# Performance work log

Hardware: AMD Instinct MI355X
Metric: run time of the kernel (lower is better)

Reference implementation:

```python
import jax, jax.numpy as jnp
import numpy as np

CONF_THRESH = 0.01
IOU_THRESH = 0.5
K = 512          # fixed pre-NMS candidate count (top-K by confidence)
MAX_WH = 4096.0  # class offset for class-aware NMS (yolov5 style)
B, N, C = 16, 25200, 85  # batch, anchors (640x640 yolov5), 5+80 classes


def xywh2xyxy(b):
    xy, wh = b[..., :2], b[..., 2:4] * 0.5
    return jnp.concatenate([xy - wh, xy + wh], axis=-1)


def box_iou(a, b):
    # a: [M,4], b: [P,4] in xyxy -> [M,P]
    lt = jnp.maximum(a[:, None, :2], b[None, :, :2])
    rb = jnp.minimum(a[:, None, 2:], b[None, :, 2:])
    inter = jnp.clip(rb - lt, 0.0).prod(-1)
    area_a = (a[:, 2] - a[:, 0]) * (a[:, 3] - a[:, 1])
    area_b = (b[:, 2] - b[:, 0]) * (b[:, 3] - b[:, 1])
    return inter / (area_a[:, None] + area_b[None, :] - inter + 1e-9)


def _score_one(pred, target):
    # pred: [N, 85] = [xywh, obj, 80 class scores]
    obj = pred[:, 4]
    cls_conf = pred[:, 5:] * obj[:, None]            # obj * class prob
    conf = cls_conf.max(-1)
    cls = jnp.argmax(cls_conf, -1)
    boxes = xywh2xyxy(pred[:, :4])
    valid = (obj > CONF_THRESH) & (conf > CONF_THRESH)
    masked = jnp.where(valid, conf, -1.0)
    scores, order = jax.lax.top_k(masked, K)          # sorted desc, fixed K
    b = boxes[order]
    c = cls[order]
    v = scores > 0.0
    # class-aware NMS via coordinate offset
    off = b + c[:, None].astype(b.dtype) * MAX_WH
    iou = box_iou(off, off)                            # [K,K]
    idxs = jnp.arange(K)

    def body(i, keep):
        sup = jnp.any((iou[i] > IOU_THRESH) & keep & (idxs < i))
        return keep.at[i].set(v[i] & ~sup)

    keep = jax.lax.fori_loop(0, K, body, jnp.zeros(K, bool))

    tmask = keep & (c == target[5].astype(jnp.int32))  # correct-class kept boxes
    iou_t = box_iou(b, target[None, :4])[:, 0]         # IoU with target box
    m = jnp.where(tmask, iou_t, -1.0)
    j = jnp.argmax(m)
    return jnp.where(jnp.any(tmask), scores[j] * iou_t[j], 0.0)


def setup_inputs() -> dict:
    key = jax.random.key(0)
    k1, k2, k3, k4 = jax.random.split(key, 4)
    xy = jax.random.uniform(k1, (B, N, 2)) * 640.0
    wh = jax.random.uniform(k2, (B, N, 2)) * 160.0 + 4.0
    obj = jax.random.uniform(k3, (B, N, 1))
    cls = jax.random.uniform(k4, (B, N, C - 5))
    x = jnp.concatenate([xy, wh, obj, cls], axis=-1)
    target = jnp.array([120.0, 150.0, 360.0, 420.0, 0.9, 17.0], dtype=jnp.float32)
    return {"x": x, "target": target}


def reference(x, target):
    return jax.vmap(lambda p: _score_one(p, target))(x)  # [B]
```

## Files before the change

kernel.cpp:

```cpp
#include <hip/hip_runtime.h>
#include <stdint.h>

#pragma clang fp contract(off)

#define BB 16
#define NN 25200
#define CCH 85
#define KTOP 512
#define NBKT 1024
#define CAP 1024


__global__ __launch_bounds__(256) void k_conf(const float* __restrict__ x,
                                              float* __restrict__ conf) {
    __shared__ float tile[128 * CCH];
    const int blk = blockIdx.x;
    const int tid = threadIdx.x;

    const float4* src = (const float4*)x + (size_t)blk * 2720;
    float4* dst = (float4*)tile;
    for (int i = tid; i < 2720; i += 256) dst[i] = src[i];
    __syncthreads();

    const int r = tid >> 1;
    const int half = tid & 1;
    const float* row = tile + r * CCH;
    const float obj = row[4];

    float best = -1.0f;
    const float* cp = row + 5 + half * 40;
#pragma unroll
    for (int j = 0; j < 40; ++j) best = fmaxf(best, cp[j] * obj);
    best = fmaxf(best, __shfl_xor(best, 1));

    if (half == 0) {
        const int gr = blk * 128 + r;
        conf[gr] = ((obj > 0.01f) && (best > 0.01f)) ? best : -1.0f;
    }
}

__global__ __launch_bounds__(1024) void k_fused(const float* __restrict__ x,
                                                const float* __restrict__ target,
                                                const float* __restrict__ conf,
                                                float* __restrict__ out) {
    __shared__ union {
        unsigned hist[NBKT];
        unsigned mask[KTOP][16];
    } um;
    __shared__ unsigned long long cand[CAP];
    __shared__ float4 sox[KTOP];
    __shared__ float sscore[KTOP];
    __shared__ unsigned keep_words[16];
    __shared__ unsigned long long wred[16];
    __shared__ int sh_tstar, sh_cnt;

    const int b = blockIdx.x;
    const int tid = threadIdx.x;
    const int lane = tid & 63;
    const float4* cb4 = (const float4*)(conf + (size_t)b * NN);

    um.hist[tid] = 0u;
    if (tid == 0) { sh_tstar = 0; sh_cnt = 0; }
    __syncthreads();
    for (int i4 = tid; i4 < NN / 4; i4 += 1024) {
        float4 c4 = cb4[i4];
        float cs[4] = {c4.x, c4.y, c4.z, c4.w};
#pragma unroll
        for (int e = 0; e < 4; ++e) {
            float c = cs[e];
            if (c > 0.0f) {
                int bk = (int)(c * 1024.0f);
                if (bk > NBKT - 1) bk = NBKT - 1;
                atomicAdd(&um.hist[bk], 1u);
            }
        }
    }
    __syncthreads();

    for (int off = 1; off < NBKT; off <<= 1) {
        unsigned v = um.hist[tid];
        if (tid + off < NBKT) v += um.hist[tid + off];
        __syncthreads();
        um.hist[tid] = v;
        __syncthreads();
    }
    if (um.hist[tid] >= KTOP && (tid == NBKT - 1 || um.hist[tid + 1] < KTOP)) sh_tstar = tid;
    __syncthreads();
    const int tstar = sh_tstar;

    for (int i4 = tid; i4 < NN / 4; i4 += 1024) {
        float4 c4 = cb4[i4];
        float cs[4] = {c4.x, c4.y, c4.z, c4.w};
#pragma unroll
        for (int e = 0; e < 4; ++e) {
            float c = cs[e];
            bool want = false;
            if (c > 0.0f) {
                int bk = (int)(c * 1024.0f);
                if (bk > NBKT - 1) bk = NBKT - 1;
                want = (bk >= tstar);
            }
            unsigned long long bal = __ballot(want);
            int base = 0;
            if (lane == 0 && bal) base = atomicAdd(&sh_cnt, __popcll(bal));
            base = __shfl(base, 0);
            if (want) {
                int pos = base + __popcll(bal & ((1ull << lane) - 1ull));
                if (pos < CAP) {
                    unsigned bits = __float_as_uint(c);
                    cand[pos] = ((unsigned long long)bits << 32) | (unsigned)(~(i4 * 4 + e));
                }
            }
        }
    }
    __syncthreads();
    const int M = min(sh_cnt, CAP);

    unsigned long long key = (tid < M) ? cand[tid] : 0ull;
    __syncthreads();
    for (int kk = 2; kk <= CAP; kk <<= 1) {
        for (int j = kk >> 1; j > 0; j >>= 1) {
            unsigned long long partner;
            if (j >= 64) {
                cand[tid] = key;
                __syncthreads();
                partner = cand[tid ^ j];
                __syncthreads();
            } else {
                partner = __shfl_xor(key, j);
            }
            bool desc = (tid & kk) == 0;
            bool lower = (tid & j) == 0;
            bool take_max = (lower == desc);
            bool pg = partner > key;
            key = (take_max == pg) ? partner : key;
        }
    }
    cand[tid] = key;
    __syncthreads();

    const int rank = tid >> 1;
    const int half = tid & 1;
    unsigned long long rkey = cand[rank];
    float sc = __uint_as_float((unsigned)(rkey >> 32));
    unsigned idx = ~((unsigned)rkey);
    const bool v = sc > 0.0f;
    float X1 = 0.f, Y1 = 0.f, X2 = 0.f, Y2 = 0.f;
    int cl = 0;
    if (v) {
        const float* rw = x + ((size_t)b * NN + idx) * CCH;
        const float obj = rw[4];
        float bbest = -1.0f;
        int bi = 0;
        const float* cp = rw + 5 + half * 40;
#pragma unroll 8
        for (int j = 0; j < 40; ++j) {
            float p = cp[j] * obj;
            if (p > bbest) { bbest = p; bi = j; }
        }
        bi += half * 40;
        float ov = __shfl_xor(bbest, 1);
        int oi = __shfl_xor(bi, 1);
        if (half == 0) {
            if (ov > bbest) { bbest = ov; bi = oi; }
            cl = bi;
            float cx = rw[0], cy = rw[1];
            float w = rw[2] * 0.5f, h = rw[3] * 0.5f;
            X1 = cx - w; Y1 = cy - h; X2 = cx + w; Y2 = cy + h;
        }
    }
    if (half == 0) {
        sscore[rank] = sc;
        float offv = (float)cl * 4096.0f;
        sox[rank] = make_float4(X1 + offv, Y1 + offv, X2 + offv, Y2 + offv);
    }
    __syncthreads();

    for (int p = tid; p < KTOP * 16; p += 1024) {
        int i = p & (KTOP - 1);
        int w = p >> 9;
        unsigned bits = 0u;
        if ((w << 5) < i) {
            float4 bi4 = sox[i];
            float ai = (bi4.z - bi4.x) * (bi4.w - bi4.y);
            const int jbase = w << 5;
            for (int jj = 0; jj < 32; ++jj) {
                int j = jbase + jj;
                float4 bj = sox[j];
                float lx = fmaxf(bi4.x, bj.x);
                float ly = fmaxf(bi4.y, bj.y);
                float rx = fminf(bi4.z, bj.z);
                float ry = fminf(bi4.w, bj.w);
                float inter = fmaxf(rx - lx, 0.0f) * fmaxf(ry - ly, 0.0f);
                float aj = (bj.z - bj.x) * (bj.w - bj.y);
                float den = ai + aj - inter + 1e-9f;
                float iou = inter / den;
                unsigned hit = (unsigned)((j < i) & (iou > 0.5f));
                bits |= hit << jj;
            }
        }
        um.mask[i][w] = bits;
    }
    __syncthreads();

    if (tid < 64) {
        const int l15 = tid & 15;
        unsigned keepw = 0u;
        unsigned r_cur = um.mask[0][l15];
        float sc_cur = sscore[0];
        for (int i = 0; i < KTOP; ++i) {
            unsigned r_next = 0u; float sc_next = 0.f;
            if (i < KTOP - 1) { r_next = um.mask[i + 1][l15]; sc_next = sscore[i + 1]; }
            unsigned long long bal = __ballot((r_cur & keepw) != 0u);
            bool sup = (bal & 0xFFFFull) != 0ull;
            bool kept = (sc_cur > 0.0f) && !sup;
            if (kept && tid == (i >> 5)) keepw |= (1u << (i & 31));
            r_cur = r_next; sc_cur = sc_next;
        }
        if (tid < 16) keep_words[tid] = keepw;
    }
    __syncthreads();

    const float tb0 = target[0], tb1 = target[1], tb2 = target[2], tb3 = target[3];
    const int tcls = (int)target[5];
    float m = -1.0f;
    if (half == 0) {
        bool kept = (keep_words[rank >> 5] >> (rank & 31)) & 1u;
        if (kept && cl == tcls) {
            float lx = fmaxf(X1, tb0);
            float ly = fmaxf(Y1, tb1);
            float rx = fminf(X2, tb2);
            float ry = fminf(Y2, tb3);
            float inter = fmaxf(rx - lx, 0.0f) * fmaxf(ry - ly, 0.0f);
            float areab = (X2 - X1) * (Y2 - Y1);
            float areat = (tb2 - tb0) * (tb3 - tb1);
            float den = areab + areat - inter + 1e-9f;
            m = inter / den;
        }
    }
    unsigned mb = __float_as_uint(m);
    unsigned mono = (mb & 0x80000000u) ? ~mb : (mb | 0x80000000u);
    unsigned long long rk = ((unsigned long long)mono << 32) | (unsigned)(~rank);
    for (int d = 32; d > 0; d >>= 1) {
        unsigned long long o = __shfl_xor(rk, d);
        if (o > rk) rk = o;
    }
    if ((tid & 63) == 0) wred[tid >> 6] = rk;
    __syncthreads();
    if (tid == 0) {
        unsigned long long bestk = wred[0];
        for (int i = 1; i < 16; ++i)
            if (wred[i] > bestk) bestk = wred[i];
        unsigned mono2 = (unsigned)(bestk >> 32);
        unsigned mbits = (mono2 & 0x80000000u) ? (mono2 & 0x7FFFFFFFu) : ~mono2;
        float mstar = __uint_as_float(mbits);
        int j = (int)(~((unsigned)bestk));
        out[b] = (mstar >= 0.0f) ? sscore[j] * mstar : 0.0f;
    }
}

extern "C" void kernel_launch(void* const* d_in, const int* in_sizes, int n_in,
                              void* d_out, int out_size, void* d_ws, size_t ws_size,
                              hipStream_t stream) {
    const float* x = (const float*)d_in[0];
    const float* target = (const float*)d_in[1];
    float* out = (float*)d_out;
    float* conf = (float*)d_ws;

    k_conf<<<dim3((BB * NN) / 128), dim3(256), 0, stream>>>(x, conf);
    k_fused<<<dim3(BB), dim3(1024), 0, stream>>>(x, target, conf, out);
}
```

Measured before the change: 316.0 us.

## Split NMS IoU-mask stage across 128 cooperative blocks with grid syncs

Replaces the 16-block fused kernel with a cooperative 128-block kernel. Phase one is top-K selection per image on 16 blocks, now with a shuffle-based histogram scan. Those blocks write boxes, scores and classes to global workspace. After a grid sync, 8 blocks per image each compute a slice of the K×K IoU suppression bitmask, reusing precomputed areas. A second grid sync hands off to the sequential greedy suppression and final target scoring, run per image with a deeper prefetch. The aim is to spread the quadratic IoU work over more CUs, at the cost of two grid-wide barriers and extra global-memory round trips.

Result: slower. 368.2 us (+16.5%).

```diff
diff --git a/kernel.cpp b/kernel.cpp
--- a/kernel.cpp
+++ b/kernel.cpp
@@ -1,4 +1,5 @@
 #include <hip/hip_runtime.h>
+#include <hip/hip_cooperative_groups.h>
 #include <stdint.h>
 
 #pragma clang fp contract(off)
@@ -10,6 +11,10 @@
 #define NBKT 1024
 #define CAP 1024
 
+#define META0 1703936
+#define SB 65536
+
+namespace cg = cooperative_groups;
 
 __global__ __launch_bounds__(256) void k_conf(const float* __restrict__ x,
                                               float* __restrict__ conf) {
@@ -39,150 +44,177 @@
     }
 }
 
-__global__ __launch_bounds__(1024) void k_fused(const float* __restrict__ x,
-                                                const float* __restrict__ target,
-                                                const float* __restrict__ conf,
-                                                float* __restrict__ out) {
+__global__ __launch_bounds__(1024) void k_rest(const float* __restrict__ x,
+                                               const float* __restrict__ target,
+                                               const float* __restrict__ conf,
+                                               char* __restrict__ meta,
+                                               float* __restrict__ out) {
     __shared__ union {
-        unsigned hist[NBKT];
+        struct { unsigned hist[NBKT]; unsigned long long cand[CAP]; } p1;
         unsigned mask[KTOP][16];
     } um;
-    __shared__ unsigned long long cand[CAP];
     __shared__ float4 sox[KTOP];
+    __shared__ float sarea[KTOP];
     __shared__ float sscore[KTOP];
+    __shared__ int scls[KTOP];
+    __shared__ unsigned wsum[16];
     __shared__ unsigned keep_words[16];
     __shared__ unsigned long long wred[16];
     __shared__ int sh_tstar, sh_cnt;
 
-    const int b = blockIdx.x;
+    cg::grid_group grid = cg::this_grid();
     const int tid = threadIdx.x;
     const int lane = tid & 63;
-    const float4* cb4 = (const float4*)(conf + (size_t)b * NN);
-
-    um.hist[tid] = 0u;
-    if (tid == 0) { sh_tstar = 0; sh_cnt = 0; }
-    __syncthreads();
-    for (int i4 = tid; i4 < NN / 4; i4 += 1024) {
-        float4 c4 = cb4[i4];
-        float cs[4] = {c4.x, c4.y, c4.z, c4.w};
+    const int bid = blockIdx.x;
+
+    if (bid < BB) {
+        const int b = bid;
+        char* mb = meta + (size_t)b * SB;
+        const float4* cb4 = (const float4*)(conf + (size_t)b * NN);
+
+        um.p1.hist[tid] = 0u;
+        if (tid == 0) { sh_tstar = 0; sh_cnt = 0; }
+        __syncthreads();
+        for (int i4 = tid; i4 < NN / 4; i4 += 1024) {
+            float4 c4 = cb4[i4];
+            float cs[4] = {c4.x, c4.y, c4.z, c4.w};
 #pragma unroll
-        for (int e = 0; e < 4; ++e) {
-            float c = cs[e];
-            if (c > 0.0f) {
-                int bk = (int)(c * 1024.0f);
-                if (bk > NBKT - 1) bk = NBKT - 1;
-                atomicAdd(&um.hist[bk], 1u);
-            }
+            for (int e = 0; e < 4; ++e) {
+                float c = cs[e];
+                if (c > 0.0f) {
+                    int bk = (int)(c * 1024.0f);
+                    if (bk > NBKT - 1) bk = NBKT - 1;
+                    atomicAdd(&um.p1.hist[bk], 1u);
+                }
+            }
+        }
+        __syncthreads();
+
+        unsigned v = um.p1.hist[tid];
+        unsigned s = v;
+#pragma unroll
+        for (int d = 1; d < 64; d <<= 1) {
+            unsigned t = __shfl_down(s, d);
+            if (lane + d < 64) s += t;
+        }
+        if (lane == 0) wsum[tid >> 6] = s;
+        __syncthreads();
+        unsigned off = 0;
+        for (int w = (tid >> 6) + 1; w < 16; ++w) off += wsum[w];
+        unsigned S = s + off;
+        if (S >= KTOP && (S - v) < KTOP) sh_tstar = tid;
+        __syncthreads();
+        const int tstar = sh_tstar;
+
+        for (int i4 = tid; i4 < NN / 4; i4 += 1024) {
+            float4 c4 = cb4[i4];
+            float cs[4] = {c4.x, c4.y, c4.z, c4.w};
+#pragma unroll
+            for (int e = 0; e < 4; ++e) {
+                float c = cs[e];
+                bool want = false;
+                if (c > 0.0f) {
+                    int bk = (int)(c * 1024.0f);
+                    if (bk > NBKT - 1) bk = NBKT - 1;
+                    want = (bk >= tstar);
+                }
+                unsigned long long bal = __ballot(want);
+                int base = 0;
+                if (lane == 0 && bal) base = atomicAdd(&sh_cnt, __popcll(bal));
+                base = __shfl(base, 0);
+                if (want) {
+                    int pos = base + __popcll(bal & ((1ull << lane) - 1ull));
+                    if (pos < CAP) {
+                        unsigned bits = __float_as_uint(c);
+                        um.p1.cand[pos] =
+                            ((unsigned long long)bits << 32) | (unsigned)(~(i4 * 4 + e));
+                    }
+                }
+            }
+        }
+        __syncthreads();
+        const int M = min(sh_cnt, CAP);
+
+        unsigned long long key = (tid < M) ? um.p1.cand[tid] : 0ull;
+        __syncthreads();
+        for (int kk = 2; kk <= CAP; kk <<= 1) {
+            for (int j = kk >> 1; j > 0; j >>= 1) {
+                unsigned long long partner;
+                if (j >= 64) {
+                    um.p1.cand[tid] = key;
+                    __syncthreads();
+                    partner = um.p1.cand[tid ^ j];
+                    __syncthreads();
+                } else {
+                    partner = __shfl_xor(key, j);
+                }
+                bool desc = (tid & kk) == 0;
+                bool lower = (tid & j) == 0;
+                bool take_max = (lower == desc);
+                bool pg = partner > key;
+                key = (take_max == pg) ? partner : key;
+            }
+        }
+        um.p1.cand[tid] = key;
+        __syncthreads();
+
+        const int rank = tid >> 1;
+        const int half = tid & 1;
+        unsigned long long rkey = um.p1.cand[rank];
+        float sc = __uint_as_float((unsigned)(rkey >> 32));
+        unsigned idx = ~((unsigned)rkey);
+        const bool v2 = sc > 0.0f;
+        float X1 = 0.f, Y1 = 0.f, X2 = 0.f, Y2 = 0.f;
+        int cl = 0;
+        if (v2) {
+            const float* rw = x + ((size_t)b * NN + idx) * CCH;
+            const float obj = rw[4];
+            float bbest = -1.0f;
+            int bi = 0;
+            const float* cp = rw + 5 + half * 40;
+#pragma unroll 8
+            for (int j = 0; j < 40; ++j) {
+                float p = cp[j] * obj;
+                if (p > bbest) { bbest = p; bi = j; }
+            }
+            bi += half * 40;
+            float ov = __shfl_xor(bbest, 1);
+            int oi = __shfl_xor(bi, 1);
+            if (half == 0) {
+                if (ov > bbest) { bbest = ov; bi = oi; }
+                cl = bi;
+                float cx = rw[0], cy = rw[1];
+                float w = rw[2] * 0.5f, h = rw[3] * 0.5f;
+                X1 = cx - w; Y1 = cy - h; X2 = cx + w; Y2 = cy + h;
+            }
+        }
+        if (half == 0) {
+            float offv = (float)cl * 4096.0f;
+            ((float4*)mb)[rank] = make_float4(X1 + offv, Y1 + offv, X2 + offv, Y2 + offv);
+            ((float4*)(mb + 8192))[rank] = make_float4(X1, Y1, X2, Y2);
+            ((float*)(mb + 16384))[rank] = sc;
+            ((int*)(mb + 18432))[rank] = cl;
         }
     }
-    __syncthreads();
-
-    for (int off = 1; off < NBKT; off <<= 1) {
-        unsigned v = um.hist[tid];
-        if (tid + off < NBKT) v += um.hist[tid + off];
-        __syncthreads();
-        um.hist[tid] = v;
-        __syncthreads();
-    }
-    if (um.hist[tid] >= KTOP && (tid == NBKT - 1 || um.hist[tid + 1] < KTOP)) sh_tstar = tid;
-    __syncthreads();
-    const int tstar = sh_tstar;
-
-    for (int i4 = tid; i4 < NN / 4; i4 += 1024) {
-        float4 c4 = cb4[i4];
-        float cs[4] = {c4.x, c4.y, c4.z, c4.w};
-#pragma unroll
-        for (int e = 0; e < 4; ++e) {
-            float c = cs[e];
-            bool want = false;
-            if (c > 0.0f) {
-                int bk = (int)(c * 1024.0f);
-                if (bk > NBKT - 1) bk = NBKT - 1;
-                want = (bk >= tstar);
-            }
-            unsigned long long bal = __ballot(want);
-            int base = 0;
-            if (lane == 0 && bal) base = atomicAdd(&sh_cnt, __popcll(bal));
-            base = __shfl(base, 0);
-            if (want) {
-                int pos = base + __popcll(bal & ((1ull << lane) - 1ull));
-                if (pos < CAP) {
-                    unsigned bits = __float_as_uint(c);
-                    cand[pos] = ((unsigned long long)bits << 32) | (unsigned)(~(i4 * 4 + e));
-                }
-            }
-        }
-    }
-    __syncthreads();
-    const int M = min(sh_cnt, CAP);
-
-    unsigned long long key = (tid < M) ? cand[tid] : 0ull;
-    __syncthreads();
-    for (int kk = 2; kk <= CAP; kk <<= 1) {
-        for (int j = kk >> 1; j > 0; j >>= 1) {
-            unsigned long long partner;
-            if (j >= 64) {
-                cand[tid] = key;
-                __syncthreads();
-                partner = cand[tid ^ j];
-                __syncthreads();
-            } else {
-                partner = __shfl_xor(key, j);
-            }
-            bool desc = (tid & kk) == 0;
-            bool lower = (tid & j) == 0;
-            bool take_max = (lower == desc);
-            bool pg = partner > key;
-            key = (take_max == pg) ? partner : key;
-        }
-    }
-    cand[tid] = key;
-    __syncthreads();
-
-    const int rank = tid >> 1;
-    const int half = tid & 1;
-    unsigned long long rkey = cand[rank];
-    float sc = __uint_as_float((unsigned)(rkey >> 32));
-    unsigned idx = ~((unsigned)rkey);
-    const bool v = sc > 0.0f;
-    float X1 = 0.f, Y1 = 0.f, X2 = 0.f, Y2 = 0.f;
-    int cl = 0;
-    if (v) {
-        const float* rw = x + ((size_t)b * NN + idx) * CCH;
-        const float obj = rw[4];
-        float bbest = -1.0f;
-        int bi = 0;
-        const float* cp = rw + 5 + half * 40;
-#pragma unroll 8
-        for (int j = 0; j < 40; ++j) {
-            float p = cp[j] * obj;
-            if (p > bbest) { bbest = p; bi = j; }
-        }
-        bi += half * 40;
-        float ov = __shfl_xor(bbest, 1);
-        int oi = __shfl_xor(bi, 1);
-        if (half == 0) {
-            if (ov > bbest) { bbest = ov; bi = oi; }
-            cl = bi;
-            float cx = rw[0], cy = rw[1];
-            float w = rw[2] * 0.5f, h = rw[3] * 0.5f;
-            X1 = cx - w; Y1 = cy - h; X2 = cx + w; Y2 = cy + h;
-        }
-    }
-    if (half == 0) {
-        sscore[rank] = sc;
-        float offv = (float)cl * 4096.0f;
-        sox[rank] = make_float4(X1 + offv, Y1 + offv, X2 + offv, Y2 + offv);
-    }
-    __syncthreads();
-
-    for (int p = tid; p < KTOP * 16; p += 1024) {
-        int i = p & (KTOP - 1);
-        int w = p >> 9;
+    __threadfence();
+    grid.sync();
+
+    {
+        const int b = bid >> 3;
+        const int slice = bid & 7;
+        char* mb = meta + (size_t)b * SB;
+        if (tid < KTOP) {
+            float4 o = ((const float4*)mb)[tid];
+            sox[tid] = o;
+            sarea[tid] = (o.z - o.x) * (o.w - o.y);
+        }
+        __syncthreads();
+        const int i = slice * 64 + (tid >> 4);
+        const int w = tid & 15;
         unsigned bits = 0u;
         if ((w << 5) < i) {
             float4 bi4 = sox[i];
-            float ai = (bi4.z - bi4.x) * (bi4.w - bi4.y);
+            float ai = sarea[i];
             const int jbase = w << 5;
             for (int jj = 0; jj < 32; ++jj) {
                 int j = jbase + jj;
@@ -192,70 +224,84 @@
                 float rx = fminf(bi4.z, bj.z);
                 float ry = fminf(bi4.w, bj.w);
                 float inter = fmaxf(rx - lx, 0.0f) * fmaxf(ry - ly, 0.0f);
-                float aj = (bj.z - bj.x) * (bj.w - bj.y);
-                float den = ai + aj - inter + 1e-9f;
+                float den = ai + sarea[j] - inter + 1e-9f;
                 float iou = inter / den;
                 unsigned hit = (unsigned)((j < i) & (iou > 0.5f));
                 bits |= hit << jj;
             }
         }
-        um.mask[i][w] = bits;
+        ((unsigned*)(mb + 20480))[slice * 1024 + tid] = bits;
     }
-    __syncthreads();
-
-    if (tid < 64) {
-        const int l15 = tid & 15;
-        unsigned keepw = 0u;
-        unsigned r_cur = um.mask[0][l15];
-        float sc_cur = sscore[0];
-        for (int i = 0; i < KTOP; ++i) {
-            unsigned r_next = 0u; float sc_next = 0.f;
-            if (i < KTOP - 1) { r_next = um.mask[i + 1][l15]; sc_next = sscore[i + 1]; }
-            unsigned long long bal = __ballot((r_cur & keepw) != 0u);
-            bool sup = (bal & 0xFFFFull) != 0ull;
-            bool kept = (sc_cur > 0.0f) && !sup;
-            if (kept && tid == (i >> 5)) keepw |= (1u << (i & 31));
-            r_cur = r_next; sc_cur = sc_next;
-        }
-        if (tid < 16) keep_words[tid] = keepw;
-    }
-    __syncthreads();
-
-    const float tb0 = target[0], tb1 = target[1], tb2 = target[2], tb3 = target[3];
-    const int tcls = (int)target[5];
-    float m = -1.0f;
-    if (half == 0) {
-        bool kept = (keep_words[rank >> 5] >> (rank & 31)) & 1u;
-        if (kept && cl == tcls) {
-            float lx = fmaxf(X1, tb0);
-            float ly = fmaxf(Y1, tb1);
-            float rx = fminf(X2, tb2);
-            float ry = fminf(Y2, tb3);
-            float inter = fmaxf(rx - lx, 0.0f) * fmaxf(ry - ly, 0.0f);
-            float areab = (X2 - X1) * (Y2 - Y1);
-            float areat = (tb2 - tb0) * (tb3 - tb1);
-            float den = areab + areat - inter + 1e-9f;
-            m = inter / den;
-        }
-    }
-    unsigned mb = __float_as_uint(m);
-    unsigned mono = (mb & 0x80000000u) ? ~mb : (mb | 0x80000000u);
-    unsigned long long rk = ((unsigned long long)mono << 32) | (unsigned)(~rank);
-    for (int d = 32; d > 0; d >>= 1) {
-        unsigned long long o = __shfl_xor(rk, d);
-        if (o > rk) rk = o;
-    }
-    if ((tid & 63) == 0) wred[tid >> 6] = rk;
-    __syncthreads();
-    if (tid == 0) {
-        unsigned long long bestk = wred[0];
-        for (int i = 1; i < 16; ++i)
-            if (wred[i] > bestk) bestk = wred[i];
-        unsigned mono2 = (unsigned)(bestk >> 32);
-        unsigned mbits = (mono2 & 0x80000000u) ? (mono2 & 0x7FFFFFFFu) : ~mono2;
-        float mstar = __uint_as_float(mbits);
-        int j = (int)(~((unsigned)bestk));
-        out[b] = (mstar >= 0.0f) ? sscore[j] * mstar : 0.0f;
+    __threadfence();
+    grid.sync();
+
+    if (bid < BB) {
+        const int b = bid;
+        const char* mb = meta + (size_t)b * SB;
+        const uint4* mg = (const uint4*)(mb + 20480);
+        for (int p = tid; p < 2048; p += 1024) ((uint4*)um.mask)[p] = mg[p];
+        if (tid < KTOP) {
+            sox[tid] = ((const float4*)(mb + 8192))[tid];
+            sscore[tid] = ((const float*)(mb + 16384))[tid];
+            scls[tid] = ((const int*)(mb + 18432))[tid];
+        }
+        __syncthreads();
+
+        if (tid < 64) {
+            const int l15 = tid & 15;
+            unsigned keepw = 0u;
+            unsigned r0 = um.mask[0][l15], r1 = um.mask[1][l15];
+            float s0 = sscore[0], s1 = sscore[1];
+            for (int i = 0; i < KTOP; ++i) {
+                unsigned r2 = 0u; float s2 = 0.f;
+                if (i < KTOP - 2) { r2 = um.mask[i + 2][l15]; s2 = sscore[i + 2]; }
+                unsigned long long bal = __ballot((r0 & keepw) != 0u);
+                bool sup = (bal & 0xFFFFull) != 0ull;
+                bool kept = (s0 > 0.0f) && !sup;
+                if (kept && tid == (i >> 5)) keepw |= (1u << (i & 31));
+                r0 = r1; r1 = r2; s0 = s1; s1 = s2;
+            }
+            if (tid < 16) keep_words[tid] = keepw;
+        }
+        __syncthreads();
+
+        const float tb0 = target[0], tb1 = target[1], tb2 = target[2], tb3 = target[3];
+        const int tcls = (int)target[5];
+        float m = -1.0f;
+        if (tid < KTOP) {
+            bool kept = (keep_words[tid >> 5] >> (tid & 31)) & 1u;
+            if (kept && scls[tid] == tcls) {
+                float4 bx = sox[tid];
+                float lx = fmaxf(bx.x, tb0);
+                float ly = fmaxf(bx.y, tb1);
+                float rx = fminf(bx.z, tb2);
+                float ry = fminf(bx.w, tb3);
+                float inter = fmaxf(rx - lx, 0.0f) * fmaxf(ry - ly, 0.0f);
+                float areab = (bx.z - bx.x) * (bx.w - bx.y);
+                float areat = (tb2 - tb0) * (tb3 - tb1);
+                float den = areab + areat - inter + 1e-9f;
+                m = inter / den;
+            }
+        }
+        unsigned mbb = __float_as_uint(m);
+        unsigned mono = (mbb & 0x80000000u) ? ~mbb : (mbb | 0x80000000u);
+        unsigned long long rk = ((unsigned long long)mono << 32) | (unsigned)(~tid);
+        for (int d = 32; d > 0; d >>= 1) {
+            unsigned long long o = __shfl_xor(rk, d);
+            if (o > rk) rk = o;
+        }
+        if ((tid & 63) == 0) wred[tid >> 6] = rk;
+        __syncthreads();
+        if (tid == 0) {
+            unsigned long long bestk = wred[0];
+            for (int i = 1; i < 16; ++i)
+                if (wred[i] > bestk) bestk = wred[i];
+            unsigned mono2 = (unsigned)(bestk >> 32);
+            unsigned mbits = (mono2 & 0x80000000u) ? (mono2 & 0x7FFFFFFFu) : ~mono2;
+            float mstar = __uint_as_float(mbits);
+            int j = (int)(~((unsigned)bestk));
+            out[b] = (mstar >= 0.0f) ? sscore[j] * mstar : 0.0f;
+        }
     }
 }
 
@@ -266,7 +312,11 @@
     const float* target = (const float*)d_in[1];
     float* out = (float*)d_out;
     float* conf = (float*)d_ws;
+    char* meta = (char*)d_ws + META0;
 
     k_conf<<<dim3((BB * NN) / 128), dim3(256), 0, stream>>>(x, conf);
-    k_fused<<<dim3(BB), dim3(1024), 0, stream>>>(x, target, conf, out);
+
+    void* args[5] = {(void*)&x, (void*)&target, (void*)&conf, (void*)&meta, (void*)&out};
+    hipLaunchCooperativeKernel(reinterpret_cast<void*>(&k_rest), dim3(128), dim3(1024),
+                               args, 0u, stream);
 }
```
